# Performance work log

Hardware: AMD Instinct MI355X
Metric: run time of the kernel (lower is better)

## Reference

```python
import jax, jax.numpy as jnp
import numpy as np
from jax import lax

FEAT_X, FEAT_Y = 50, 37          # generate_anchors(50, 37)
BASE_SIZE, DSR = 8.0, 16.0
A = FEAT_X * FEAT_Y * 9          # 16650 anchors


def generate_anchors():
    # Vectorized version of the triple python loop; order: x, y, size, [b1,b2,b3]
    xs = jnp.arange(FEAT_X, dtype=jnp.float32)[:, None, None]
    ys = jnp.arange(FEAT_Y, dtype=jnp.float32)[None, :, None]
    s = jnp.array([BASE_SIZE, 2 * BASE_SIZE, 4 * BASE_SIZE], jnp.float32)[None, None, :]

    def box(x1, y1, x2, y2):
        return jnp.stack(jnp.broadcast_arrays(x1 * DSR, y1 * DSR, x2 * DSR, y2 * DSR), axis=-1)

    b1 = box(xs - s / 2, ys - s / 2, xs + s / 2, ys + s / 2)      # square
    b2 = box(xs - s,     ys - s / 4, xs + s,     ys + s / 4)      # wide
    b3 = box(xs - s / 4, ys - s,     xs + s / 4, ys + s)          # tall
    anchors = jnp.stack([b1, b2, b3], axis=3)  # (50,37,3 sizes,3 variants,4)
    return anchors.reshape(-1, 4)              # (16650,4)


def conv2d(x, w, b, padding):
    y = lax.conv_general_dilated(x, w, (1, 1), padding,
                                 dimension_numbers=("NCHW", "OIHW", "NCHW"))
    return y + b[None, :, None, None]


def pairwise_iou(anchors, gt):
    # anchors: (A,4), gt: (B,G,4) -> iou (B,A,G); zero when no positive overlap
    a = anchors[None, :, None, :]
    g = gt[:, None, :, :]
    area_a = (a[..., 2] - a[..., 0]) * (a[..., 3] - a[..., 1])
    area_g = (g[..., 2] - g[..., 0]) * (g[..., 3] - g[..., 1])
    left = jnp.maximum(a[..., 0], g[..., 0])
    right = jnp.minimum(a[..., 2], g[..., 2])
    top = jnp.maximum(a[..., 1], g[..., 1])
    bot = jnp.minimum(a[..., 3], g[..., 3])
    no_ov = (left >= right) | (top >= bot)
    inter = jnp.where(no_ov, 0.0, (right - left) * (bot - top))
    return jnp.where(no_ov, 0.0, inter / (area_a + area_g - inter))


def setup_inputs() -> dict:
    key = jax.random.key(0)
    k1, k2, k3, k4, k5, k6, k7, k8 = jax.random.split(key, 8)
    B, G = 8, 20
    feats = jax.random.normal(k1, (B, 512, FEAT_Y, FEAT_X), jnp.float32)
    # well-formed gt boxes inside an ~800x592 image
    raw = jax.random.uniform(k2, (B, G, 2, 2)) * jnp.array([800.0, 592.0])
    x1y1 = jnp.min(raw, axis=2)
    x2y2 = jnp.max(raw, axis=2) + 1.0
    gt_boxes = jnp.concatenate([x1y1, x2y2], axis=-1)  # (B,G,4)
    im_info = jnp.array([[592.0, 800.0, 1.0]], jnp.float32)  # (h, w, scale)
    s = 0.02
    w3 = jax.random.normal(k3, (512, 512, 3, 3), jnp.float32) * s
    b3 = jnp.zeros((512,), jnp.float32)
    wc = jax.random.normal(k4, (18, 512, 1, 1), jnp.float32) * s
    bc = jnp.zeros((18,), jnp.float32)
    wb = jax.random.normal(k5, (36, 512, 1, 1), jnp.float32) * s
    bb = jnp.zeros((36,), jnp.float32)
    return {"feats": feats, "w3": w3, "b3": b3, "wc": wc, "bc": bc,
            "wb": wb, "bb": bb, "gt_boxes": gt_boxes, "im_info": im_info}


def reference(feats, w3, b3, wc, bc, wb, bb, gt_boxes, im_info):
    B = feats.shape[0]
    anchors = generate_anchors()
    rpn_conv1 = jax.nn.relu(conv2d(feats, w3, b3, ((1, 1), (1, 1))))
    rpn_cls_score = conv2d(rpn_conv1, wc, bc, ((0, 0), (0, 0)))  # (B,18,H,W)
    Bc, C, H, W = rpn_cls_score.shape
    score_rs = rpn_cls_score.reshape(Bc, 2, (C * H) // 2, W)      # reshape(x, 2)
    rpn_cls_prob = jax.nn.softmax(score_rs, axis=1).reshape(Bc, 18, H, W)
    rpn_bbox_pred = conv2d(rpn_conv1, wb, bb, ((0, 0), (0, 0)))   # (B,36,H,W)

    # anchor-target assignment (training branch), faithful to original logic
    inside = ((anchors[:, 0] >= 0) & (anchors[:, 1] >= 0) &
              (anchors[:, 2] < im_info[0, 1]) & (anchors[:, 3] < im_info[0, 0]))
    iou = pairwise_iou(anchors, gt_boxes)                 # (B,A,G)
    iou = jnp.where(inside[None, :, None], iou, 0.0)      # outside anchors skipped
    G = gt_boxes.shape[1]
    # original: idxs = argmax(iou_matrix[:][j]) with j == last gt index
    idx = jnp.argmax(iou[:, G - 1, :], axis=-1)           # (B,)
    labels = jnp.zeros((B, anchors.shape[0]), jnp.float32)
    labels = labels.at[jnp.arange(B), idx].set(1.0)
    max_iou = jnp.max(iou, axis=-1)                       # (B,A)
    labels = jnp.where(inside[None, :] & (max_iou > 0.7), 0.0, labels)

    out = jnp.concatenate([rpn_cls_prob, rpn_bbox_pred], axis=1)  # (B,54,H,W)
    return out, iou, labels
```

## Files before the change

### kernel.cpp

```cpp
#include <hip/hip_runtime.h>

typedef unsigned short u16;
typedef unsigned int u32;
typedef float f32x4 __attribute__((ext_vector_type(4)));
typedef short bf16x8 __attribute__((ext_vector_type(8)));

#define NB 8
#define FH 37
#define FW 50
#define FHW 1850
#define MTOT 14800
#define CIN 512
#define KTOT 4608
#define HP 39
#define WP 52
#define ANCH 16650
#define NG 20

#define ZB 356
#define WTB 512
#define WHB 128
#define TRB 3712
#define PRE_TOT (ZB + WTB + WHB + TRB)

#define CONVB 960
#define IOB 528

__device__ __forceinline__ u16 f2bf(float f) {
    u32 u = __float_as_uint(f);
    u += 0x7fffu + ((u >> 16) & 1u);
    return (u16)(u >> 16);
}

__device__ __forceinline__ void gl2lds16(const u16* g, u16* l) {
    __builtin_amdgcn_global_load_lds((const __attribute__((address_space(1))) void*)(g),
                                     (__attribute__((address_space(3))) void*)(l),
                                     16, 0, 0);
}

__device__ __forceinline__ void anchor_box(int a, float& x1, float& y1, float& x2, float& y2) {
    int x = a / 333;
    int rem = a - x * 333;
    int y = rem / 9;
    int r2 = rem - y * 9;
    int si = r2 / 3;
    int bi = r2 - si * 3;
    float s = (float)(8 << si);
    float fx = (float)x, fy = (float)y;
    float ax1, ay1, ax2, ay2;
    if (bi == 0)      { float h = s * 0.5f;  ax1 = fx - h; ay1 = fy - h; ax2 = fx + h; ay2 = fy + h; }
    else if (bi == 1) { float q = s * 0.25f; ax1 = fx - s; ay1 = fy - q; ax2 = fx + s; ay2 = fy + q; }
    else              { float q = s * 0.25f; ax1 = fx - q; ay1 = fy - s; ax2 = fx + q; ay2 = fy + s; }
    x1 = ax1 * 16.f; y1 = ay1 * 16.f; x2 = ax2 * 16.f; y2 = ay2 * 16.f;
}

__global__ __launch_bounds__(256) void k_pre(u16* __restrict__ apad,
                                             const float* __restrict__ w3, u16* __restrict__ wt,
                                             const float* __restrict__ wc, const float* __restrict__ wb,
                                             u16* __restrict__ whd,
                                             const float* __restrict__ feats) {
    __shared__ __attribute__((aligned(16))) char smraw[18432];
    int blk = blockIdx.x;
    int t = threadIdx.x;

    if (blk < ZB) {
        uint4* apad4 = (uint4*)apad;
        int i = blk * 256 + t;
        int img = i / 11392;
        int r = i - img * 11392;
        int u4;
        if (r < 3328) u4 = r;
        else if (r < 6656) u4 = 126464 + (r - 3328);
        else {
            int rp = r - 6656;
            int h = 1 + (rp >> 7);
            int c2 = rp & 127;
            int col = (c2 & 64) ? 51 : 0;
            u4 = (h * 52 + col) * 64 + (c2 & 63);
        }
        apad4[img * 129792 + u4] = make_uint4(0u, 0u, 0u, 0u);
    } else if (blk < ZB + WTB) {
        float* lt = (float*)smraw;
        int n = blk - ZB;
        const float* src = w3 + n * KTOT;
        for (int i = t; i < KTOT; i += 256) lt[i] = src[i];
        __syncthreads();
        u16* dst = wt + n * KTOT;
        for (int o = t; o < KTOT; o += 256) {
            int tap = o >> 9, ci = o & 511;
            dst[o] = f2bf(lt[ci * 9 + tap]);
        }
    } else if (blk < ZB + WTB + WHB) {
        int i = (blk - ZB - WTB) * 256 + t;
        int n = i >> 9;
        int ci = i & 511;
        float v = 0.f;
        if (n < 18) v = wc[n * 512 + ci];
        else if (n < 54) v = wb[(n - 18) * 512 + ci];
        whd[i] = f2bf(v);
    } else {
        float* tile = (float*)smraw;
        int q = blk - ZB - WTB - WHB;
        int xt = q % 58;
        int r2 = q / 58;
        int ct = r2 & 7;
        int img = r2 >> 3;
        int hw0 = xt * 32, c0 = ct * 64;
        int lx = t & 31, ly = t >> 5;
        #pragma unroll
        for (int rr = 0; rr < 8; rr++) {
            int cl = ly + rr * 8;
            int hw = hw0 + lx;
            if (hw < FHW) tile[cl * 33 + lx] = feats[(img * 512 + c0 + cl) * FHW + hw];
        }
        __syncthreads();
        #pragma unroll
        for (int rr = 0; rr < 4; rr++) {
            int hwl = ly + rr * 8;
            int hw2 = hw0 + hwl;
            if (hw2 < FHW) {
                int h = hw2 / FW, w = hw2 - h * FW;
                float v0 = tile[(2 * lx) * 33 + hwl];
                float v1 = tile[(2 * lx + 1) * 33 + hwl];
                u32 pk = (u32)f2bf(v0) | ((u32)f2bf(v1) << 16);
                u32* dst = (u32*)&apad[(((img * HP) + h + 1) * WP + (w + 1)) * 512 + c0];
                dst[lx] = pk;
            }
        }
    }
}

__global__ __launch_bounds__(256) void k_conv(const u16* __restrict__ apad,
                                              const u16* __restrict__ wt,
                                              const float* __restrict__ b3,
                                              u16* __restrict__ act,
                                              const float* __restrict__ gt,
                                              const float* __restrict__ im,
                                              float* __restrict__ iou_out,
                                              float* __restrict__ lab) {
    __shared__ __attribute__((aligned(16))) char sm[24576];
    __shared__ int idxs;
    int L = blockIdx.x;
    int tid = threadIdx.x;

    if (L < CONVB) {
        u16* As = (u16*)sm;
        u16* Bs = (u16*)(sm + 16384);
        int mb = (L & 7) + 8 * (L >> 6);
        int nb = (L >> 3) & 7;
        if (mb >= 116) return;
        int wave = tid >> 6, lane = tid & 63;
        int m0 = mb * 128;
        int n0 = nb * 64;
        int wr = wave >> 1, wn = wave & 1;
        int lm = lane & 15, lq = lane >> 4;
        int l7 = lm & 7;

        f32x4 acc[4][2] = {};

        int rloc = tid >> 3;
        int cg = (tid & 7) ^ (rloc & 7);
        int aBase[4], bBase[2];
        for (int i = 0; i < 4; i++) {
            int m = m0 + i * 32 + rloc; if (m > MTOT - 1) m = MTOT - 1;
            int b = m / FHW; int hw = m - b * FHW;
            int h = hw / FW; int w = hw - h * FW;
            aBase[i] = ((b * HP + h) * WP + w) * 512 + cg * 8;
        }
        for (int j = 0; j < 2; j++)
            bBase[j] = (n0 + j * 32 + rloc) * KTOT + cg * 8;

        u16* aL[4]; u16* bL[2];
        for (int i = 0; i < 4; i++) aL[i] = &As[(i * 32 + wave * 8) * 64];
        for (int j = 0; j < 2; j++) bL[j] = &Bs[(j * 32 + wave * 8) * 64];

        for (int kk = 0; kk < KTOT; kk += 64) {
            int tap = kk >> 9;
            int ci0 = kk & 511;
            int dy = tap / 3, dx = tap - dy * 3;
            int aOfs = (dy * WP + dx) * 512 + ci0;
            gl2lds16(apad + aBase[0] + aOfs, aL[0]);
            gl2lds16(apad + aBase[1] + aOfs, aL[1]);
            gl2lds16(apad + aBase[2] + aOfs, aL[2]);
            gl2lds16(apad + aBase[3] + aOfs, aL[3]);
            gl2lds16(wt + bBase[0] + kk, bL[0]);
            gl2lds16(wt + bBase[1] + kk, bL[1]);
            __syncthreads();
            bf16x8 a[2][4], b[2][2];
            #pragma unroll
            for (int ks = 0; ks < 2; ks++) {
                int slotb = ((ks * 4 + lq) ^ l7) * 8;
                #pragma unroll
                for (int i = 0; i < 4; i++)
                    a[ks][i] = *(const bf16x8*)&As[(wr * 64 + i * 16 + lm) * 64 + slotb];
                #pragma unroll
                for (int j = 0; j < 2; j++)
                    b[ks][j] = *(const bf16x8*)&Bs[(wn * 32 + j * 16 + lm) * 64 + slotb];
            }
            #pragma unroll
            for (int ks = 0; ks < 2; ks++)
                #pragma unroll
                for (int i = 0; i < 4; i++)
                    #pragma unroll
                    for (int j = 0; j < 2; j++)
                        acc[i][j] = __builtin_amdgcn_mfma_f32_16x16x32_bf16(a[ks][i], b[ks][j], acc[i][j], 0, 0, 0);
            __syncthreads();
        }

        for (int j = 0; j < 2; j++) {
            int n = n0 + wn * 32 + j * 16 + lm;
            float bias = b3[n];
            for (int i = 0; i < 4; i++) {
                int mb2 = m0 + wr * 64 + i * 16 + lq * 4;
                for (int r = 0; r < 4; r++) {
                    int m = mb2 + r;
                    if (m < MTOT) {
                        float v = acc[i][j][r] + bias;
                        act[m * 512 + n] = f2bf(v > 0.f ? v : 0.f);
                    }
                }
            }
        }
    } else {
        float* g4 = (float*)sm;
        float* imv = g4 + 80;
        float* buf = g4 + 84;
        int q = L - CONVB;
        int at = q % 66;
        int b = q / 66;
        int t = tid;
        if (t < NG * 4) g4[t] = gt[b * NG * 4 + t];
        if (t < 2) imv[t] = im[t];
        __syncthreads();
        if (t == 0) {
            float x1, y1, x2, y2;
            anchor_box(19, x1, y1, x2, y2);
            bool inside = (x1 >= 0.f) && (y1 >= 0.f) && (x2 < imv[1]) && (y2 < imv[0]);
            float aa = (x2 - x1) * (y2 - y1);
            float best = -1.f; int bg = 0;
            for (int g2 = 0; g2 < NG; g2++) {
                float gx1 = g4[g2 * 4], gy1 = g4[g2 * 4 + 1], gx2 = g4[g2 * 4 + 2], gy2 = g4[g2 * 4 + 3];
                float l = fmaxf(x1, gx1), r = fminf(x2, gx2);
                float tp = fmaxf(y1, gy1), bo = fminf(y2, gy2);
                float v = 0.f;
                if (l < r && tp < bo) {
                    float inter = (r - l) * (bo - tp);
                    float ag = (gx2 - gx1) * (gy2 - gy1);
                    v = inter / (aa + ag - inter);
                }
                if (!inside) v = 0.f;
                if (v > best) { best = v; bg = g2; }
            }
            idxs = bg;
        }
        int a0 = at * 256;
        int a = a0 + t;
        float mx = 0.f;
        bool inside = false;
        if (a < ANCH) {
            float x1, y1, x2, y2;
            anchor_box(a, x1, y1, x2, y2);
            inside = (x1 >= 0.f) && (y1 >= 0.f) && (x2 < imv[1]) && (y2 < imv[0]);
            float aa = (x2 - x1) * (y2 - y1);
            for (int g2 = 0; g2 < NG; g2++) {
                float gx1 = g4[g2 * 4], gy1 = g4[g2 * 4 + 1], gx2 = g4[g2 * 4 + 2], gy2 = g4[g2 * 4 + 3];
                float l = fmaxf(x1, gx1), r = fminf(x2, gx2);
                float tp = fmaxf(y1, gy1), bo = fminf(y2, gy2);
                float v = 0.f;
                if (l < r && tp < bo) {
                    float inter = (r - l) * (bo - tp);
                    float ag = (gx2 - gx1) * (gy2 - gy1);
                    v = inter / (aa + ag - inter);
                }
                if (!inside) v = 0.f;
                buf[t * NG + g2] = v;
                mx = fmaxf(mx, v);
            }
        }
        __syncthreads();
        int rem = ANCH - a0;
        int cnt2 = (rem < 256 ? rem : 256) * NG;
        float* dst = iou_out + (b * ANCH + a0) * NG;
        for (int i = t; i < cnt2; i += 256) dst[i] = buf[i];
        if (a < ANCH) {
            float lv = (a == idxs) ? 1.f : 0.f;
            if (inside && mx > 0.7f) lv = 0.f;
            lab[b * ANCH + a] = lv;
        }
    }
}

__global__ __launch_bounds__(256) void k_post(const u16* __restrict__ act,
                                              const u16* __restrict__ whd,
                                              const float* __restrict__ bc,
                                              const float* __restrict__ bb,
                                              float* __restrict__ out) {
    __shared__ float Sl[4 * 16 * 65];
    int tid = threadIdx.x;
    int wave = tid >> 6, lane = tid & 63;
    int lm = lane & 15, lq = lane >> 4;
    int m0 = blockIdx.x * 64 + wave * 16;
    int mr = m0 + lm; if (mr > MTOT - 1) mr = MTOT - 1;
    const u16* arow = act + mr * 512;
    f32x4 acc[4] = {};
    for (int kk = 0; kk < 512; kk += 32) {
        bf16x8 a = *(const bf16x8*)&arow[kk + lq * 8];
        #pragma unroll
        for (int j = 0; j < 4; j++) {
            bf16x8 b = *(const bf16x8*)&whd[(j * 16 + lm) * 512 + kk + lq * 8];
            acc[j] = __builtin_amdgcn_mfma_f32_16x16x32_bf16(a, b, acc[j], 0, 0, 0);
        }
    }
    float* S = &Sl[wave * 1040];
    #pragma unroll
    for (int r = 0; r < 4; r++)
        #pragma unroll
        for (int j = 0; j < 4; j++)
            S[(lq * 4 + r) * 65 + j * 16 + lm] = acc[j][r];
    __syncthreads();
    int r16 = lane & 15, cg = lane >> 4;
    int m = m0 + r16;
    if (m < MTOT) {
        int b = m / FHW, hw = m - b * FHW;
        const float* Sr = &S[r16 * 65];
        #pragma unroll
        for (int k = 0; k < 14; k++) {
            int c = cg + 4 * k;
            if (c >= 54) break;
            float v;
            if (c < 18) {
                int c0 = c < 9 ? c : c - 9;
                float s0 = Sr[c0] + bc[c0];
                float s1 = Sr[c0 + 9] + bc[c0 + 9];
                float mx = fmaxf(s0, s1);
                float e0 = __expf(s0 - mx), e1 = __expf(s1 - mx);
                v = (c < 9 ? e0 : e1) / (e0 + e1);
            } else {
                v = Sr[c] + bb[c - 18];
            }
            out[(b * 54 + c) * FHW + hw] = v;
        }
    }
}

extern "C" void kernel_launch(void* const* d_in, const int* in_sizes, int n_in,
                              void* d_out, int out_size, void* d_ws, size_t ws_size,
                              hipStream_t stream) {
    (void)in_sizes; (void)n_in; (void)out_size; (void)ws_size;
    const float* feats = (const float*)d_in[0];
    const float* w3    = (const float*)d_in[1];
    const float* b3    = (const float*)d_in[2];
    const float* wc    = (const float*)d_in[3];
    const float* bc    = (const float*)d_in[4];
    const float* wb    = (const float*)d_in[5];
    const float* bb    = (const float*)d_in[6];
    const float* gt    = (const float*)d_in[7];
    const float* im    = (const float*)d_in[8];
    float* out = (float*)d_out;
    char* ws = (char*)d_ws;

    u16* apad = (u16*)(ws);
    u16* wt   = (u16*)(ws + 16613376);
    u16* whd  = (u16*)(ws + 21331968);
    u16* act  = (u16*)(ws + 21397504);

    float* iou_out = out + 799200;
    float* lab     = out + 3463200;

    k_pre<<<dim3(PRE_TOT), dim3(256), 0, stream>>>(apad, w3, wt, wc, wb, whd, feats);
    k_conv<<<dim3(CONVB + IOB), dim3(256), 0, stream>>>(apad, wt, b3, act, gt, im, iou_out, lab);
    k_post<<<dim3(232), dim3(256), 0, stream>>>(act, whd, bc, bb, out);
}
```

Before: 200.4 us.

## Move IoU work to prep kernel, register-prefetch conv weights, split post K

The IoU/label blocks move from the conv kernel into the preprocessing kernel, so the conv launch only runs GEMM tiles. In the conv GEMM, weight tiles are no longer staged through LDS; each lane loads its B fragments straight from global into registers and prefetches the next K step, which shrinks LDS use and may raise occupancy. The 1x1 head kernel splits K across two waves per row group and reduces the halves in shared memory, doubling the block count to spread work over more CUs. The cost is more register pressure and uncoalesced per-lane global weight reads in the conv loop.

Result: slower. 327.6 us (+63.5%).

```diff
diff --git a/kernel.cpp b/kernel.cpp
--- a/kernel.cpp
+++ b/kernel.cpp
@@ -21,10 +21,10 @@
 #define WTB 512
 #define WHB 128
 #define TRB 3712
-#define PRE_TOT (ZB + WTB + WHB + TRB)
+#define IOB 528
+#define PRE_TOT (ZB + WTB + WHB + TRB + IOB)
 
 #define CONVB 960
-#define IOB 528
 
 __device__ __forceinline__ u16 f2bf(float f) {
     u32 u = __float_as_uint(f);
@@ -58,8 +58,11 @@
                                              const float* __restrict__ w3, u16* __restrict__ wt,
                                              const float* __restrict__ wc, const float* __restrict__ wb,
                                              u16* __restrict__ whd,
-                                             const float* __restrict__ feats) {
-    __shared__ __attribute__((aligned(16))) char smraw[18432];
+                                             const float* __restrict__ feats,
+                                             const float* __restrict__ gt, const float* __restrict__ im,
+                                             float* __restrict__ iou_out, float* __restrict__ lab) {
+    __shared__ __attribute__((aligned(16))) char smraw[20864];
+    __shared__ int idxs;
     int blk = blockIdx.x;
     int t = threadIdx.x;
 
@@ -98,7 +101,7 @@
         if (n < 18) v = wc[n * 512 + ci];
         else if (n < 54) v = wb[(n - 18) * 512 + ci];
         whd[i] = f2bf(v);
-    } else {
+    } else if (blk < ZB + WTB + WHB + TRB) {
         float* tile = (float*)smraw;
         int q = blk - ZB - WTB - WHB;
         int xt = q % 58;
@@ -127,108 +130,13 @@
                 dst[lx] = pk;
             }
         }
-    }
-}
-
-__global__ __launch_bounds__(256) void k_conv(const u16* __restrict__ apad,
-                                              const u16* __restrict__ wt,
-                                              const float* __restrict__ b3,
-                                              u16* __restrict__ act,
-                                              const float* __restrict__ gt,
-                                              const float* __restrict__ im,
-                                              float* __restrict__ iou_out,
-                                              float* __restrict__ lab) {
-    __shared__ __attribute__((aligned(16))) char sm[24576];
-    __shared__ int idxs;
-    int L = blockIdx.x;
-    int tid = threadIdx.x;
-
-    if (L < CONVB) {
-        u16* As = (u16*)sm;
-        u16* Bs = (u16*)(sm + 16384);
-        int mb = (L & 7) + 8 * (L >> 6);
-        int nb = (L >> 3) & 7;
-        if (mb >= 116) return;
-        int wave = tid >> 6, lane = tid & 63;
-        int m0 = mb * 128;
-        int n0 = nb * 64;
-        int wr = wave >> 1, wn = wave & 1;
-        int lm = lane & 15, lq = lane >> 4;
-        int l7 = lm & 7;
-
-        f32x4 acc[4][2] = {};
-
-        int rloc = tid >> 3;
-        int cg = (tid & 7) ^ (rloc & 7);
-        int aBase[4], bBase[2];
-        for (int i = 0; i < 4; i++) {
-            int m = m0 + i * 32 + rloc; if (m > MTOT - 1) m = MTOT - 1;
-            int b = m / FHW; int hw = m - b * FHW;
-            int h = hw / FW; int w = hw - h * FW;
-            aBase[i] = ((b * HP + h) * WP + w) * 512 + cg * 8;
-        }
-        for (int j = 0; j < 2; j++)
-            bBase[j] = (n0 + j * 32 + rloc) * KTOT + cg * 8;
-
-        u16* aL[4]; u16* bL[2];
-        for (int i = 0; i < 4; i++) aL[i] = &As[(i * 32 + wave * 8) * 64];
-        for (int j = 0; j < 2; j++) bL[j] = &Bs[(j * 32 + wave * 8) * 64];
-
-        for (int kk = 0; kk < KTOT; kk += 64) {
-            int tap = kk >> 9;
-            int ci0 = kk & 511;
-            int dy = tap / 3, dx = tap - dy * 3;
-            int aOfs = (dy * WP + dx) * 512 + ci0;
-            gl2lds16(apad + aBase[0] + aOfs, aL[0]);
-            gl2lds16(apad + aBase[1] + aOfs, aL[1]);
-            gl2lds16(apad + aBase[2] + aOfs, aL[2]);
-            gl2lds16(apad + aBase[3] + aOfs, aL[3]);
-            gl2lds16(wt + bBase[0] + kk, bL[0]);
-            gl2lds16(wt + bBase[1] + kk, bL[1]);
-            __syncthreads();
-            bf16x8 a[2][4], b[2][2];
-            #pragma unroll
-            for (int ks = 0; ks < 2; ks++) {
-                int slotb = ((ks * 4 + lq) ^ l7) * 8;
-                #pragma unroll
-                for (int i = 0; i < 4; i++)
-                    a[ks][i] = *(const bf16x8*)&As[(wr * 64 + i * 16 + lm) * 64 + slotb];
-                #pragma unroll
-                for (int j = 0; j < 2; j++)
-                    b[ks][j] = *(const bf16x8*)&Bs[(wn * 32 + j * 16 + lm) * 64 + slotb];
-            }
-            #pragma unroll
-            for (int ks = 0; ks < 2; ks++)
-                #pragma unroll
-                for (int i = 0; i < 4; i++)
-                    #pragma unroll
-                    for (int j = 0; j < 2; j++)
-                        acc[i][j] = __builtin_amdgcn_mfma_f32_16x16x32_bf16(a[ks][i], b[ks][j], acc[i][j], 0, 0, 0);
-            __syncthreads();
-        }
-
-        for (int j = 0; j < 2; j++) {
-            int n = n0 + wn * 32 + j * 16 + lm;
-            float bias = b3[n];
-            for (int i = 0; i < 4; i++) {
-                int mb2 = m0 + wr * 64 + i * 16 + lq * 4;
-                for (int r = 0; r < 4; r++) {
-                    int m = mb2 + r;
-                    if (m < MTOT) {
-                        float v = acc[i][j][r] + bias;
-                        act[m * 512 + n] = f2bf(v > 0.f ? v : 0.f);
-                    }
-                }
-            }
-        }
     } else {
-        float* g4 = (float*)sm;
+        float* g4 = (float*)smraw;
         float* imv = g4 + 80;
         float* buf = g4 + 84;
-        int q = L - CONVB;
+        int q = blk - ZB - WTB - WHB - TRB;
         int at = q % 66;
         int b = q / 66;
-        int t = tid;
         if (t < NG * 4) g4[t] = gt[b * NG * 4 + t];
         if (t < 2) imv[t] = im[t];
         __syncthreads();
@@ -290,20 +198,127 @@
     }
 }
 
+__global__ __launch_bounds__(256) void k_conv(const u16* __restrict__ apad,
+                                              const u16* __restrict__ wt,
+                                              const float* __restrict__ b3,
+                                              u16* __restrict__ act) {
+    __shared__ __attribute__((aligned(16))) u16 As[128 * 64];
+    int L = blockIdx.x;
+    int tid = threadIdx.x;
+
+    int mb = (L & 7) + 8 * (L >> 6);
+    int nb = (L >> 3) & 7;
+    if (mb >= 116) return;
+    int wave = tid >> 6, lane = tid & 63;
+    int m0 = mb * 128;
+    int n0 = nb * 64;
+    int wr = wave >> 1, wn = wave & 1;
+    int lm = lane & 15, lq = lane >> 4;
+    int l7 = lm & 7;
+    int lqo = lq * 8;
+
+    f32x4 acc[4][2] = {};
+
+    int rloc = tid >> 3;
+    int cg = (tid & 7) ^ (rloc & 7);
+    int aBase[4];
+    for (int i = 0; i < 4; i++) {
+        int m = m0 + i * 32 + rloc; if (m > MTOT - 1) m = MTOT - 1;
+        int b = m / FHW; int hw = m - b * FHW;
+        int h = hw / FW; int w = hw - h * FW;
+        aBase[i] = ((b * HP + h) * WP + w) * 512 + cg * 8;
+    }
+    int bRow[2];
+    for (int j = 0; j < 2; j++)
+        bRow[j] = (n0 + wn * 32 + j * 16 + lm) * KTOT + lqo;
+
+    u16* aL[4];
+    for (int i = 0; i < 4; i++) aL[i] = &As[(i * 32 + wave * 8) * 64];
+
+    bf16x8 bNxt[2][2];
+    #pragma unroll
+    for (int ks = 0; ks < 2; ks++)
+        #pragma unroll
+        for (int j = 0; j < 2; j++)
+            bNxt[ks][j] = *(const bf16x8*)&wt[bRow[j] + ks * 32];
+
+    for (int kk = 0; kk < KTOT; kk += 64) {
+        bf16x8 bCur[2][2];
+        #pragma unroll
+        for (int ks = 0; ks < 2; ks++)
+            #pragma unroll
+            for (int j = 0; j < 2; j++)
+                bCur[ks][j] = bNxt[ks][j];
+
+        int tap = kk >> 9;
+        int ci0 = kk & 511;
+        int dy = tap / 3, dx = tap - dy * 3;
+        int aOfs = (dy * WP + dx) * 512 + ci0;
+        gl2lds16(apad + aBase[0] + aOfs, aL[0]);
+        gl2lds16(apad + aBase[1] + aOfs, aL[1]);
+        gl2lds16(apad + aBase[2] + aOfs, aL[2]);
+        gl2lds16(apad + aBase[3] + aOfs, aL[3]);
+
+        int kn = kk + 64;
+        if (kn < KTOT) {
+            #pragma unroll
+            for (int ks = 0; ks < 2; ks++)
+                #pragma unroll
+                for (int j = 0; j < 2; j++)
+                    bNxt[ks][j] = *(const bf16x8*)&wt[bRow[j] + kn + ks * 32];
+        }
+        __syncthreads();
+
+        bf16x8 a[2][4];
+        #pragma unroll
+        for (int ks = 0; ks < 2; ks++) {
+            int slotb = ((ks * 4 + lq) ^ l7) * 8;
+            #pragma unroll
+            for (int i = 0; i < 4; i++)
+                a[ks][i] = *(const bf16x8*)&As[(wr * 64 + i * 16 + lm) * 64 + slotb];
+        }
+        #pragma unroll
+        for (int ks = 0; ks < 2; ks++)
+            #pragma unroll
+            for (int i = 0; i < 4; i++)
+                #pragma unroll
+                for (int j = 0; j < 2; j++)
+                    acc[i][j] = __builtin_amdgcn_mfma_f32_16x16x32_bf16(a[ks][i], bCur[ks][j], acc[i][j], 0, 0, 0);
+        __syncthreads();
+    }
+
+    for (int j = 0; j < 2; j++) {
+        int n = n0 + wn * 32 + j * 16 + lm;
+        float bias = b3[n];
+        for (int i = 0; i < 4; i++) {
+            int mb2 = m0 + wr * 64 + i * 16 + lq * 4;
+            for (int r = 0; r < 4; r++) {
+                int m = mb2 + r;
+                if (m < MTOT) {
+                    float v = acc[i][j][r] + bias;
+                    act[m * 512 + n] = f2bf(v > 0.f ? v : 0.f);
+                }
+            }
+        }
+    }
+}
+
 __global__ __launch_bounds__(256) void k_post(const u16* __restrict__ act,
                                               const u16* __restrict__ whd,
                                               const float* __restrict__ bc,
                                               const float* __restrict__ bb,
                                               float* __restrict__ out) {
-    __shared__ float Sl[4 * 16 * 65];
-    int tid = threadIdx.x;
-    int wave = tid >> 6, lane = tid & 63;
-    int lm = lane & 15, lq = lane >> 4;
-    int m0 = blockIdx.x * 64 + wave * 16;
-    int mr = m0 + lm; if (mr > MTOT - 1) mr = MTOT - 1;
+    __shared__ float Sl[4][16][68];
+    int t = threadIdx.x;
+    int wave = t >> 6, lane = t & 63, lm = lane & 15, lq = lane >> 4;
+    int g = wave >> 1, kh = wave & 1;
+    int m0 = blockIdx.x * 32;
+    int mr = m0 + g * 16 + lm; if (mr > MTOT - 1) mr = MTOT - 1;
     const u16* arow = act + mr * 512;
     f32x4 acc[4] = {};
-    for (int kk = 0; kk < 512; kk += 32) {
+    #pragma unroll
+    for (int s = 0; s < 8; s++) {
+        int kk = kh * 256 + s * 32;
         bf16x8 a = *(const bf16x8*)&arow[kk + lq * 8];
         #pragma unroll
         for (int j = 0; j < 4; j++) {
@@ -311,35 +326,31 @@
             acc[j] = __builtin_amdgcn_mfma_f32_16x16x32_bf16(a, b, acc[j], 0, 0, 0);
         }
     }
-    float* S = &Sl[wave * 1040];
     #pragma unroll
     for (int r = 0; r < 4; r++)
         #pragma unroll
         for (int j = 0; j < 4; j++)
-            S[(lq * 4 + r) * 65 + j * 16 + lm] = acc[j][r];
+            Sl[wave][lq * 4 + r][j * 16 + lm] = acc[j][r];
     __syncthreads();
-    int r16 = lane & 15, cg = lane >> 4;
-    int m = m0 + r16;
-    if (m < MTOT) {
+
+    for (int i = t; i < 32 * 54; i += 256) {
+        int row = i & 31, cc = i >> 5;
+        int m = m0 + row;
+        if (m >= MTOT) continue;
+        int g2 = (row >> 4) * 2, rl = row & 15;
+        float v;
+        if (cc < 18) {
+            int c0 = cc < 9 ? cc : cc - 9;
+            float s0 = Sl[g2][rl][c0] + Sl[g2 + 1][rl][c0] + bc[c0];
+            float s1 = Sl[g2][rl][c0 + 9] + Sl[g2 + 1][rl][c0 + 9] + bc[c0 + 9];
+            float mx = fmaxf(s0, s1);
+            float e0 = __expf(s0 - mx), e1 = __expf(s1 - mx);
+            v = (cc < 9 ? e0 : e1) / (e0 + e1);
+        } else {
+            v = Sl[g2][rl][cc] + Sl[g2 + 1][rl][cc] + bb[cc - 18];
+        }
         int b = m / FHW, hw = m - b * FHW;
-        const float* Sr = &S[r16 * 65];
-        #pragma unroll
-        for (int k = 0; k < 14; k++) {
-            int c = cg + 4 * k;
-            if (c >= 54) break;
-            float v;
-            if (c < 18) {
-                int c0 = c < 9 ? c : c - 9;
-                float s0 = Sr[c0] + bc[c0];
-                float s1 = Sr[c0 + 9] + bc[c0 + 9];
-                float mx = fmaxf(s0, s1);
-                float e0 = __expf(s0 - mx), e1 = __expf(s1 - mx);
-                v = (c < 9 ? e0 : e1) / (e0 + e1);
-            } else {
-                v = Sr[c] + bb[c - 18];
-            }
-            out[(b * 54 + c) * FHW + hw] = v;
-        }
+        out[(b * 54 + cc) * FHW + hw] = v;
     }
 }
 
@@ -367,7 +378,8 @@
     float* iou_out = out + 799200;
     float* lab     = out + 3463200;
 
-    k_pre<<<dim3(PRE_TOT), dim3(256), 0, stream>>>(apad, w3, wt, wc, wb, whd, feats);
-    k_conv<<<dim3(CONVB + IOB), dim3(256), 0, stream>>>(apad, wt, b3, act, gt, im, iou_out, lab);
-    k_post<<<dim3(232), dim3(256), 0, stream>>>(act, whd, bc, bb, out);
-}
+    k_pre<<<dim3(PRE_TOT), dim3(256), 0, stream>>>(apad, w3, wt, wc, wb, whd, feats,
+                                                   gt, im, iou_out, lab);
+    k_conv<<<dim3(CONVB), dim3(256), 0, stream>>>(apad, wt, b3, act);
+    k_post<<<dim3(463), dim3(256), 0, stream>>>(act, whd, bc, bb, out);
+}
```

## Double-buffer LDS tiles in conv GEMM to overlap loads with MFMA

Applied to the files above, without the earlier changes.

Splits the A and B shared-memory tiles of the implicit-GEMM convolution into two ping-pong buffers. The global-to-LDS copies for the next K-slice are issued before the current slice's LDS reads and MFMAs, so memory latency can overlap with compute, and one barrier per step is dropped. The cost is doubled LDS use per block (48 KB instead of 24 KB), which may reduce how many blocks fit on each CU.

Result: slower. 226.2 us (+12.9%).

```diff
diff --git a/kernel.cpp b/kernel.cpp
--- a/kernel.cpp
+++ b/kernel.cpp
@@ -138,14 +138,16 @@
                                               const float* __restrict__ im,
                                               float* __restrict__ iou_out,
                                               float* __restrict__ lab) {
-    __shared__ __attribute__((aligned(16))) char sm[24576];
+    __shared__ __attribute__((aligned(16))) char sm[49152];
     __shared__ int idxs;
     int L = blockIdx.x;
     int tid = threadIdx.x;
 
     if (L < CONVB) {
-        u16* As = (u16*)sm;
-        u16* Bs = (u16*)(sm + 16384);
+        u16* As0 = (u16*)sm;
+        u16* As1 = (u16*)(sm + 16384);
+        u16* Bs0 = (u16*)(sm + 32768);
+        u16* Bs1 = (u16*)(sm + 40960);
         int mb = (L & 7) + 8 * (L >> 6);
         int nb = (L >> 3) & 7;
         if (mb >= 116) return;
@@ -170,32 +172,33 @@
         for (int j = 0; j < 2; j++)
             bBase[j] = (n0 + j * 32 + rloc) * KTOT + cg * 8;
 
-        u16* aL[4]; u16* bL[2];
-        for (int i = 0; i < 4; i++) aL[i] = &As[(i * 32 + wave * 8) * 64];
-        for (int j = 0; j < 2; j++) bL[j] = &Bs[(j * 32 + wave * 8) * 64];
-
-        for (int kk = 0; kk < KTOT; kk += 64) {
-            int tap = kk >> 9;
-            int ci0 = kk & 511;
+        int wo = wave * 8 * 64;
+
+        auto issue = [&](int kkn, u16* WA, u16* WB) {
+            int tap = kkn >> 9;
+            int ci0 = kkn & 511;
             int dy = tap / 3, dx = tap - dy * 3;
             int aOfs = (dy * WP + dx) * 512 + ci0;
-            gl2lds16(apad + aBase[0] + aOfs, aL[0]);
-            gl2lds16(apad + aBase[1] + aOfs, aL[1]);
-            gl2lds16(apad + aBase[2] + aOfs, aL[2]);
-            gl2lds16(apad + aBase[3] + aOfs, aL[3]);
-            gl2lds16(wt + bBase[0] + kk, bL[0]);
-            gl2lds16(wt + bBase[1] + kk, bL[1]);
-            __syncthreads();
+            gl2lds16(apad + aBase[0] + aOfs, &WA[wo]);
+            gl2lds16(apad + aBase[1] + aOfs, &WA[wo + 2048]);
+            gl2lds16(apad + aBase[2] + aOfs, &WA[wo + 4096]);
+            gl2lds16(apad + aBase[3] + aOfs, &WA[wo + 6144]);
+            gl2lds16(wt + bBase[0] + kkn, &WB[wo]);
+            gl2lds16(wt + bBase[1] + kkn, &WB[wo + 2048]);
+        };
+        auto step = [&](int kk, const u16* RA, const u16* RB, u16* WA, u16* WB) {
+            int kn = kk + 64;
+            if (kn < KTOT) issue(kn, WA, WB);
             bf16x8 a[2][4], b[2][2];
             #pragma unroll
             for (int ks = 0; ks < 2; ks++) {
                 int slotb = ((ks * 4 + lq) ^ l7) * 8;
                 #pragma unroll
                 for (int i = 0; i < 4; i++)
-                    a[ks][i] = *(const bf16x8*)&As[(wr * 64 + i * 16 + lm) * 64 + slotb];
+                    a[ks][i] = *(const bf16x8*)&RA[(wr * 64 + i * 16 + lm) * 64 + slotb];
                 #pragma unroll
                 for (int j = 0; j < 2; j++)
-                    b[ks][j] = *(const bf16x8*)&Bs[(wn * 32 + j * 16 + lm) * 64 + slotb];
+                    b[ks][j] = *(const bf16x8*)&RB[(wn * 32 + j * 16 + lm) * 64 + slotb];
             }
             #pragma unroll
             for (int ks = 0; ks < 2; ks++)
@@ -205,6 +208,13 @@
                     for (int j = 0; j < 2; j++)
                         acc[i][j] = __builtin_amdgcn_mfma_f32_16x16x32_bf16(a[ks][i], b[ks][j], acc[i][j], 0, 0, 0);
             __syncthreads();
+        };
+
+        issue(0, As0, Bs0);
+        __syncthreads();
+        for (int kk = 0; kk < KTOT; kk += 128) {
+            step(kk,      As0, Bs0, As1, Bs1);
+            step(kk + 64, As1, Bs1, As0, Bs0);
         }
 
         for (int j = 0; j < 2; j++) {
```
